# Performance work log

Measured on AMD Instinct MI355X. Metric: run time of the kernel, lower is better.

The kernel has to match this reference:

```python
import jax, jax.numpy as jnp
import numpy as np

D, P, H, FF, HD = 1024, 512, 16, 4096, 64
B, L = 2, 1024
EPS = 1e-5


def rotate_half(x):
    x1, x2 = jnp.split(x, 2, axis=-1)
    return jnp.concatenate([-x2, x1], axis=-1)


def apply_rope(x, pos):  # x: [B,H,L,HD], pos: [L,HD] angles
    c = jnp.cos(pos)[None, None]
    s = jnp.sin(pos)[None, None]
    return x * c + rotate_half(x) * s


def layer_norm(x, g, b):
    mu = jnp.mean(x, axis=-1, keepdims=True)
    var = jnp.var(x, axis=-1, keepdims=True)
    return (x - mu) * jax.lax.rsqrt(var + EPS) * g + b


def heads(x):  # [B,L,D] -> [B,H,L,HD]
    Bq, Lq, _ = x.shape
    return x.reshape(Bq, Lq, H, HD).transpose(0, 2, 1, 3)


def attention(q, k, v, alibi, pos, mask):
    if pos is not None:
        q = apply_rope(q, pos)
        k = apply_rope(k, pos)
    scores = jnp.einsum('bhqd,bhkd->bhqk', q, k) * (HD ** -0.5)
    scores = jnp.where(mask[:, None, None, :], -jnp.inf, scores)
    scores = scores + alibi[None]
    w = jax.nn.softmax(scores, axis=-1)
    out = jnp.einsum('bhqk,bhkd->bhqd', w, v)
    return out.transpose(0, 2, 1, 3).reshape(out.shape[0], out.shape[2], D)


def setup_inputs() -> dict:
    key = jax.random.key(0)
    ks = iter(jax.random.split(key, 64))

    def rn(shape, scale=1.0):
        return jax.random.normal(next(ks), shape, dtype=jnp.float32) * scale

    inp = {
        'memory': rn((B, L, D)),
        'tgt': rn((B, L, D)),
        'self_alibi_bias': rn((H, L, L)),
        'self_pos_emb': rn((L, HD)),
        'cross_alibi_bias': rn((H, L, L)),
        'cross_pos_emb': rn((L, HD)),
        'mask': jax.random.randint(next(ks), (B, L), 0, 2) > 0,
        # self attention params
        'sa_lat_w': rn((D, P), 0.02), 'sa_lat_b': jnp.zeros((P,)),
        'sa_q_w': rn((P, D), 0.02), 'sa_q_b': jnp.zeros((D,)),
        'sa_k_w': rn((P, D), 0.02), 'sa_k_b': jnp.zeros((D,)),
        'sa_v_w': rn((P, D), 0.02), 'sa_v_b': jnp.zeros((D,)),
        'sa_out_w': rn((D, D), 0.02), 'sa_out_b': jnp.zeros((D,)),
        # cross attention params
        'ca_lat_w': rn((D, P), 0.02), 'ca_lat_b': jnp.zeros((P,)),
        'ca_q_w': rn((D, D), 0.02), 'ca_q_b': jnp.zeros((D,)),
        'ca_k_w': rn((P, D), 0.02), 'ca_k_b': jnp.zeros((D,)),
        'ca_v_w': rn((P, D), 0.02), 'ca_v_b': jnp.zeros((D,)),
        'ca_out_w': rn((D, D), 0.02), 'ca_out_b': jnp.zeros((D,)),
        # ffn + norms
        'lin1_w': rn((D, FF), 0.02), 'lin1_b': jnp.zeros((FF,)),
        'lin2_w': rn((FF, D), 0.02), 'lin2_b': jnp.zeros((D,)),
        'n1_g': jnp.ones((D,)), 'n1_b': jnp.zeros((D,)),
        'n2_g': jnp.ones((D,)), 'n2_b': jnp.zeros((D,)),
        'n3_g': jnp.ones((D,)), 'n3_b': jnp.zeros((D,)),
    }
    return inp


def reference(memory, tgt, self_alibi_bias, self_pos_emb, cross_alibi_bias,
              cross_pos_emb, mask,
              sa_lat_w, sa_lat_b, sa_q_w, sa_q_b, sa_k_w, sa_k_b,
              sa_v_w, sa_v_b, sa_out_w, sa_out_b,
              ca_lat_w, ca_lat_b, ca_q_w, ca_q_b, ca_k_w, ca_k_b,
              ca_v_w, ca_v_b, ca_out_w, ca_out_b,
              lin1_w, lin1_b, lin2_w, lin2_b,
              n1_g, n1_b, n2_g, n2_b, n3_g, n3_b):
    # self attention (q,k,v all from latent projection of tgt)
    proj = tgt @ sa_lat_w + sa_lat_b                      # [B,L,P]
    q = heads(proj @ sa_q_w + sa_q_b)
    k = heads(proj @ sa_k_w + sa_k_b)
    v = heads(proj @ sa_v_w + sa_v_b)
    sa = attention(q, k, v, self_alibi_bias, self_pos_emb, mask)
    sa = sa @ sa_out_w + sa_out_b
    x = tgt + layer_norm(sa, n1_g, n1_b)

    # cross attention (q from current tgt stream, k/v from latent of memory)
    mproj = memory @ ca_lat_w + ca_lat_b                  # [B,L,P]
    q = heads(x @ ca_q_w + ca_q_b)
    k = heads(mproj @ ca_k_w + ca_k_b)
    v = heads(mproj @ ca_v_w + ca_v_b)
    ca = attention(q, k, v, cross_alibi_bias, cross_pos_emb, mask)
    ca = ca @ ca_out_w + ca_out_b
    x = x + layer_norm(ca, n2_g, n2_b)

    # FFN
    f = jax.nn.gelu(x @ lin1_w + lin1_b, approximate=False) @ lin2_w + lin2_b
    x = layer_norm(x + f, n3_g, n3_b)
    return x
```

## Files before the change

### kernel.cpp

```cpp
#include <hip/hip_runtime.h>
#include <hip/hip_bf16.h>
#include <math.h>

typedef __hip_bfloat16 hbf16;
typedef __attribute__((ext_vector_type(8))) short bf16x8;
typedef __attribute__((ext_vector_type(4))) float f32x4;

constexpr int kD  = 1024;
constexpr int kP  = 512;
constexpr int kH  = 16;
constexpr int kFF = 4096;
constexpr int kHD = 64;
constexpr int kB  = 2;
constexpr int kL  = 1024;
constexpr int kTok = kB * kL;

__device__ inline short f2bf(float x) { hbf16 h = __float2bfloat16(x); return *(short*)&h; }

__global__ __launch_bounds__(256) void transpose_bf16(
    const float* __restrict__ src, short* __restrict__ dst, int K, int N)
{
    __shared__ float t[32][33];
    int n0 = blockIdx.x * 32, k0 = blockIdx.y * 32;
    int tx = threadIdx.x & 31, ty = threadIdx.x >> 5;
    #pragma unroll
    for (int r = ty; r < 32; r += 8)
        t[r][tx] = src[(size_t)(k0 + r) * N + n0 + tx];
    __syncthreads();
    #pragma unroll
    for (int r = ty; r < 32; r += 8)
        dst[(size_t)(n0 + r) * K + k0 + tx] = f2bf(t[tx][r]);
}

__global__ __launch_bounds__(256) void bias_fill(
    const float* __restrict__ bias, float* __restrict__ C, int N, int total4)
{
    int i = blockIdx.x * 256 + threadIdx.x;
    if (i >= total4) return;
    int n = (i * 4) & (N - 1);
    *(float4*)&C[(size_t)i * 4] = *(const float4*)&bias[n];
}

__global__ void concat_bias(float* __restrict__ o, const float* __restrict__ a,
                            const float* __restrict__ b, const float* __restrict__ c, int n)
{
    int i = blockIdx.x * blockDim.x + threadIdx.x;
    if (i < n) o[i] = a[i];
    else if (i < 2 * n) { if (b) o[i] = b[i - n]; }
    else if (i < 3 * n) { if (c) o[i] = c[i - 2 * n]; }
}

constexpr int LDK = 40;
__global__ __launch_bounds__(256) void gemm_mfma(
    const float* __restrict__ A, const short* __restrict__ WT,
    const float* __restrict__ bias, float* __restrict__ C,
    int M, int N, int K, int act, int ksplit)
{
    __shared__ short As[128 * LDK];
    __shared__ short Bs[128 * LDK];
    const int tid = threadIdx.x;
    const int m0 = blockIdx.y * 128, n0 = blockIdx.x * 128;
    const int ks = K / ksplit;
    const int kbeg = blockIdx.z * ks, kend = kbeg + ks;
    const int wave = tid >> 6, lane = tid & 63;
    const int wm = (wave & 1) * 64, wn = (wave >> 1) * 64;
    const int l15 = lane & 15, quad = lane >> 4;

    const int am = tid >> 3, akq = (tid & 7) * 4;
    const int bn = tid >> 2, bkg = (tid & 3) * 8;

    f32x4 acc[4][4];
    #pragma unroll
    for (int i = 0; i < 4; ++i)
        #pragma unroll
        for (int j = 0; j < 4; ++j)
            acc[i][j] = (f32x4){0.f, 0.f, 0.f, 0.f};

    float4 ra[4];
    bf16x8 rb[2];
    #pragma unroll
    for (int e = 0; e < 4; ++e)
        ra[e] = *(const float4*)&A[(size_t)(m0 + am + e * 32) * K + kbeg + akq];
    #pragma unroll
    for (int e = 0; e < 2; ++e)
        rb[e] = *(const bf16x8*)&WT[(size_t)(n0 + bn + e * 64) * K + kbeg + bkg];

    for (int kk = kbeg; kk < kend; kk += 32) {
        #pragma unroll
        for (int e = 0; e < 4; ++e) {
            short4 s4 = make_short4(f2bf(ra[e].x), f2bf(ra[e].y), f2bf(ra[e].z), f2bf(ra[e].w));
            *(short4*)&As[(am + e * 32) * LDK + akq] = s4;
        }
        #pragma unroll
        for (int e = 0; e < 2; ++e)
            *(bf16x8*)&Bs[(bn + e * 64) * LDK + bkg] = rb[e];
        __syncthreads();

        if (kk + 32 < kend) {
            #pragma unroll
            for (int e = 0; e < 4; ++e)
                ra[e] = *(const float4*)&A[(size_t)(m0 + am + e * 32) * K + kk + 32 + akq];
            #pragma unroll
            for (int e = 0; e < 2; ++e)
                rb[e] = *(const bf16x8*)&WT[(size_t)(n0 + bn + e * 64) * K + kk + 32 + bkg];
        }

        bf16x8 af[4], bfr[4];
        #pragma unroll
        for (int i = 0; i < 4; ++i)
            af[i] = *(bf16x8*)&As[(wm + i * 16 + l15) * LDK + quad * 8];
        #pragma unroll
        for (int j = 0; j < 4; ++j)
            bfr[j] = *(bf16x8*)&Bs[(wn + j * 16 + l15) * LDK + quad * 8];
        #pragma unroll
        for (int i = 0; i < 4; ++i)
            #pragma unroll
            for (int j = 0; j < 4; ++j)
                acc[i][j] = __builtin_amdgcn_mfma_f32_16x16x32_bf16(af[i], bfr[j], acc[i][j], 0, 0, 0);
        __syncthreads();
    }

    #pragma unroll
    for (int j = 0; j < 4; ++j) {
        int n = n0 + wn + j * 16 + l15;
        if (ksplit == 1) {
            float bv = bias[n];
            #pragma unroll
            for (int i = 0; i < 4; ++i) {
                int mb = m0 + wm + i * 16 + quad * 4;
                #pragma unroll
                for (int r = 0; r < 4; ++r) {
                    float v = acc[i][j][r] + bv;
                    if (act) v = v * 0.5f * (1.0f + erff(v * 0.70710678118654752f));
                    C[(size_t)(mb + r) * N + n] = v;
                }
            }
        } else {
            #pragma unroll
            for (int i = 0; i < 4; ++i) {
                int mb = m0 + wm + i * 16 + quad * 4;
                #pragma unroll
                for (int r = 0; r < 4; ++r)
                    atomicAdd(&C[(size_t)(mb + r) * N + n], acc[i][j][r]);
            }
        }
    }
}

__global__ void qk_pack(const float* __restrict__ x, const float* __restrict__ pos,
                        short* __restrict__ outp, float scale, int ldx, int off)
{
    int idx = blockIdx.x * blockDim.x + threadIdx.x;
    if (idx >= kTok * kH * 32) return;
    int d = idx & 31;
    int h = (idx >> 5) & (kH - 1);
    int row = idx >> 9;
    int l = row & (kL - 1);
    int b = row >> 10;
    float a1 = pos[l * kHD + d];
    float a2 = pos[l * kHD + d + 32];
    size_t base = (size_t)row * ldx + off + h * kHD;
    float x1 = x[base + d], x2 = x[base + d + 32];
    float r1 = (x1 * cosf(a1) - x2 * sinf(a1)) * scale;
    float r2 = (x2 * cosf(a2) + x1 * sinf(a2)) * scale;
    size_t ob = ((size_t)(b * kH + h) * kL + l) * 64;
    outp[ob + d]      = f2bf(r1);
    outp[ob + d + 32] = f2bf(r2);
}

__global__ __launch_bounds__(256) void v_pack(const float* __restrict__ v, short* __restrict__ outp,
                                              int ldx, int off)
{
    int l0 = blockIdx.x * 64, h = blockIdx.y, b = blockIdx.z;
    __shared__ float t[64][65];
    int tid = threadIdx.x;
    #pragma unroll
    for (int e = 0; e < 4; ++e) {
        int idx = tid + e * 256;
        int r = idx >> 4, c4 = (idx & 15) * 4;
        const float4 vv = *(const float4*)&v[(size_t)(b * kL + l0 + r) * ldx + off + h * kHD + c4];
        t[r][c4] = vv.x; t[r][c4 + 1] = vv.y; t[r][c4 + 2] = vv.z; t[r][c4 + 3] = vv.w;
    }
    __syncthreads();
    int hd = tid >> 2, seg = (tid & 3) * 16;
    size_t ob = ((size_t)(b * kH + h) * 64 + hd) * kL + l0 + seg;
    short tmp[16];
    #pragma unroll
    for (int i = 0; i < 16; ++i) tmp[i] = f2bf(t[seg + i][hd]);
    #pragma unroll
    for (int i = 0; i < 16; i += 4)
        *(short4*)&outp[ob + i] = make_short4(tmp[i], tmp[i + 1], tmp[i + 2], tmp[i + 3]);
}

constexpr int AQ = 64, AK = 64;
constexpr int QLD = 72;
constexpr int PLD = 68;
__global__ __launch_bounds__(256) void attn_mfma(
    const short* __restrict__ qpk, const short* __restrict__ kpk,
    const short* __restrict__ vpk, const float* __restrict__ alibi,
    const int* __restrict__ mask, float* __restrict__ out)
{
    const int q0 = blockIdx.x * AQ, h = blockIdx.y, b = blockIdx.z;
    const int tid = threadIdx.x, wave = tid >> 6, lane = tid & 63;
    const int l15 = lane & 15, quad = lane >> 4;
    __shared__ short Qs[AQ * QLD];
    __shared__ short Ks[AK * QLD];
    __shared__ short Vt[kHD * QLD];
    __shared__ float Ps[AQ * PLD];

    const short* qbase = qpk + ((size_t)(b * kH + h) * kL) * 64;
    const short* kbase = kpk + ((size_t)(b * kH + h) * kL) * 64;
    const short* vbase = vpk + ((size_t)(b * kH + h) * 64) * kL;

    #pragma unroll
    for (int e = 0; e < 2; ++e) {
        int idx = tid + e * 256;
        int r = idx >> 3, c8 = (idx & 7) * 8;
        *(bf16x8*)&Qs[r * QLD + c8] = *(const bf16x8*)&qbase[(size_t)(q0 + r) * 64 + c8];
    }
    float mst[4], lst[4];
    #pragma unroll
    for (int r = 0; r < 4; ++r) { mst[r] = -3e38f; lst[r] = 0.f; }
    f32x4 oacc[4];
    #pragma unroll
    for (int j = 0; j < 4; ++j) oacc[j] = (f32x4){0.f, 0.f, 0.f, 0.f};
    __syncthreads();

    for (int k0 = 0; k0 < kL; k0 += AK) {
        #pragma unroll
        for (int e = 0; e < 2; ++e) {
            int idx = tid + e * 256;
            int r = idx >> 3, c8 = (idx & 7) * 8;
            *(bf16x8*)&Ks[r * QLD + c8] = *(const bf16x8*)&kbase[(size_t)(k0 + r) * 64 + c8];
            *(bf16x8*)&Vt[r * QLD + c8] = *(const bf16x8*)&vbase[(size_t)r * kL + k0 + c8];
        }
        __syncthreads();

        bf16x8 aq[2];
        #pragma unroll
        for (int s = 0; s < 2; ++s)
            aq[s] = *(bf16x8*)&Qs[(wave * 16 + l15) * QLD + s * 32 + quad * 8];
        f32x4 sacc[4];
        #pragma unroll
        for (int nt = 0; nt < 4; ++nt) sacc[nt] = (f32x4){0.f, 0.f, 0.f, 0.f};
        #pragma unroll
        for (int nt = 0; nt < 4; ++nt)
            #pragma unroll
            for (int s = 0; s < 2; ++s) {
                bf16x8 bk = *(bf16x8*)&Ks[(nt * 16 + l15) * QLD + s * 32 + quad * 8];
                sacc[nt] = __builtin_amdgcn_mfma_f32_16x16x32_bf16(aq[s], bk, sacc[nt], 0, 0, 0);
            }

        float sv[4][4];
        float mx[4] = {-3e38f, -3e38f, -3e38f, -3e38f};
        #pragma unroll
        for (int nt = 0; nt < 4; ++nt) {
            int key = k0 + nt * 16 + l15;
            int mk = mask[b * kL + key];
            #pragma unroll
            for (int r = 0; r < 4; ++r) {
                int qrow = q0 + wave * 16 + quad * 4 + r;
                float al = alibi[((size_t)h * kL + qrow) * kL + key];
                float s = mk ? -1e30f : sacc[nt][r];
                s += al;
                sv[nt][r] = s;
                mx[r] = fmaxf(mx[r], s);
            }
        }
        #pragma unroll
        for (int m = 1; m <= 8; m <<= 1)
            #pragma unroll
            for (int r = 0; r < 4; ++r)
                mx[r] = fmaxf(mx[r], __shfl_xor(mx[r], m));
        float alpha[4], lsum[4];
        #pragma unroll
        for (int r = 0; r < 4; ++r) {
            float mn = fmaxf(mst[r], mx[r]);
            alpha[r] = __expf(mst[r] - mn);
            mst[r] = mn;
            lsum[r] = 0.f;
        }
        #pragma unroll
        for (int nt = 0; nt < 4; ++nt)
            #pragma unroll
            for (int r = 0; r < 4; ++r) {
                float p = __expf(sv[nt][r] - mst[r]);
                sv[nt][r] = p;
                lsum[r] += p;
            }
        #pragma unroll
        for (int m = 1; m <= 8; m <<= 1)
            #pragma unroll
            for (int r = 0; r < 4; ++r)
                lsum[r] += __shfl_xor(lsum[r], m);
        #pragma unroll
        for (int r = 0; r < 4; ++r) lst[r] = lst[r] * alpha[r] + lsum[r];

        #pragma unroll
        for (int nt = 0; nt < 4; ++nt)
            #pragma unroll
            for (int r = 0; r < 4; ++r)
                Ps[(wave * 16 + quad * 4 + r) * PLD + nt * 16 + l15] = sv[nt][r];
        #pragma unroll
        for (int j = 0; j < 4; ++j)
            #pragma unroll
            for (int r = 0; r < 4; ++r)
                oacc[j][r] *= alpha[r];
        __syncthreads();

        #pragma unroll
        for (int s = 0; s < 2; ++s) {
            const float* pr = &Ps[(wave * 16 + l15) * PLD + s * 32 + quad * 8];
            float4 p0 = *(const float4*)&pr[0];
            float4 p1 = *(const float4*)&pr[4];
            bf16x8 ap;
            ap[0] = f2bf(p0.x); ap[1] = f2bf(p0.y); ap[2] = f2bf(p0.z); ap[3] = f2bf(p0.w);
            ap[4] = f2bf(p1.x); ap[5] = f2bf(p1.y); ap[6] = f2bf(p1.z); ap[7] = f2bf(p1.w);
            #pragma unroll
            for (int j = 0; j < 4; ++j) {
                bf16x8 bv = *(bf16x8*)&Vt[(j * 16 + l15) * QLD + s * 32 + quad * 8];
                oacc[j] = __builtin_amdgcn_mfma_f32_16x16x32_bf16(ap, bv, oacc[j], 0, 0, 0);
            }
        }
        __syncthreads();
    }

    #pragma unroll
    for (int j = 0; j < 4; ++j)
        #pragma unroll
        for (int r = 0; r < 4; ++r) {
            int qrow = q0 + wave * 16 + quad * 4 + r;
            out[(size_t)(b * kL + qrow) * kD + h * kHD + j * 16 + l15] = oacc[j][r] / lst[r];
        }
}

__global__ __launch_bounds__(256) void add_ln(
    const float* __restrict__ res, const float* __restrict__ z,
    const float* __restrict__ g, const float* __restrict__ bi,
    float* __restrict__ out)
{
    int row = blockIdx.x, tid = threadIdx.x;
    __shared__ float red[256], red2[256];
    const float* zr = z + (size_t)row * kD;
    float s = 0.f, sq = 0.f;
    for (int i = tid; i < kD; i += 256) { float vv = zr[i]; s += vv; sq += vv * vv; }
    red[tid] = s; red2[tid] = sq; __syncthreads();
    for (int st = 128; st > 0; st >>= 1) {
        if (tid < st) { red[tid] += red[tid + st]; red2[tid] += red2[tid + st]; }
        __syncthreads();
    }
    float mean = red[0] / kD;
    float var = red2[0] / kD - mean * mean;
    float rstd = rsqrtf(var + 1e-5f);
    for (int i = tid; i < kD; i += 256) {
        float vv = (zr[i] - mean) * rstd * g[i] + bi[i];
        out[(size_t)row * kD + i] = res[(size_t)row * kD + i] + vv;
    }
}

__global__ __launch_bounds__(256) void ln_final(
    const float* __restrict__ res, const float* __restrict__ f,
    const float* __restrict__ g, const float* __restrict__ bi,
    float* __restrict__ out)
{
    int row = blockIdx.x, tid = threadIdx.x;
    __shared__ float tt[kD];
    __shared__ float red[256], red2[256];
    float s = 0.f, sq = 0.f;
    for (int i = tid; i < kD; i += 256) {
        float vv = res[(size_t)row * kD + i] + f[(size_t)row * kD + i];
        tt[i] = vv; s += vv; sq += vv * vv;
    }
    red[tid] = s; red2[tid] = sq; __syncthreads();
    for (int st = 128; st > 0; st >>= 1) {
        if (tid < st) { red[tid] += red[tid + st]; red2[tid] += red2[tid + st]; }
        __syncthreads();
    }
    float mean = red[0] / kD;
    float var = red2[0] / kD - mean * mean;
    float rstd = rsqrtf(var + 1e-5f);
    for (int i = tid; i < kD; i += 256)
        out[(size_t)row * kD + i] = (tt[i] - mean) * rstd * g[i] + bi[i];
}

extern "C" void kernel_launch(void* const* d_in, const int* in_sizes, int n_in,
                              void* d_out, int out_size, void* d_ws, size_t ws_size,
                              hipStream_t stream)
{
    const float* memory      = (const float*)d_in[0];
    const float* tgt         = (const float*)d_in[1];
    const float* self_alibi  = (const float*)d_in[2];
    const float* self_pos    = (const float*)d_in[3];
    const float* cross_alibi = (const float*)d_in[4];
    const float* cross_pos   = (const float*)d_in[5];
    const int*   mask        = (const int*)d_in[6];
    const float* sa_lat_w = (const float*)d_in[7];   const float* sa_lat_b = (const float*)d_in[8];
    const float* sa_q_w   = (const float*)d_in[9];   const float* sa_q_b   = (const float*)d_in[10];
    const float* sa_k_w   = (const float*)d_in[11];  const float* sa_k_b   = (const float*)d_in[12];
    const float* sa_v_w   = (const float*)d_in[13];  const float* sa_v_b   = (const float*)d_in[14];
    const float* sa_out_w = (const float*)d_in[15];  const float* sa_out_b = (const float*)d_in[16];
    const float* ca_lat_w = (const float*)d_in[17];  const float* ca_lat_b = (const float*)d_in[18];
    const float* ca_q_w   = (const float*)d_in[19];  const float* ca_q_b   = (const float*)d_in[20];
    const float* ca_k_w   = (const float*)d_in[21];  const float* ca_k_b   = (const float*)d_in[22];
    const float* ca_v_w   = (const float*)d_in[23];  const float* ca_v_b   = (const float*)d_in[24];
    const float* ca_out_w = (const float*)d_in[25];  const float* ca_out_b = (const float*)d_in[26];
    const float* lin1_w   = (const float*)d_in[27];  const float* lin1_b   = (const float*)d_in[28];
    const float* lin2_w   = (const float*)d_in[29];  const float* lin2_b   = (const float*)d_in[30];
    const float* n1_g = (const float*)d_in[31];  const float* n1_b = (const float*)d_in[32];
    const float* n2_g = (const float*)d_in[33];  const float* n2_b = (const float*)d_in[34];
    const float* n3_g = (const float*)d_in[35];  const float* n3_b = (const float*)d_in[36];

    const size_t M1 = 1u << 20;
    float* W     = (float*)d_ws;
    float* xb    = W + 0 * M1;
    float* tmp   = W + 2 * M1;
    float* proj  = W + 4 * M1;
    float* qkvb  = W + 5 * M1;
    float* attnb = W + 11 * M1;
    float* ffh   = W + 4 * M1;
    short* wslot = (short*)(W + 13 * M1);
    float* bcat  = W + 11 * M1;
    short* qpk = (short*)(W + 2 * M1);
    short* kpk = (short*)(W + 3 * M1);
    short* vpk = (short*)(W + 4 * M1);

    auto gemm = [&](const float* A, const float* Wt, const float* bias, float* C,
                    int M, int N, int K, int act, int S) {
        transpose_bf16<<<dim3(N / 32, K / 32), dim3(256), 0, stream>>>(Wt, wslot, K, N);
        if (S > 1)
            bias_fill<<<dim3(M * N / 1024), dim3(256), 0, stream>>>(bias, C, N, M * N / 4);
        gemm_mfma<<<dim3(N / 128, M / 128, S), dim3(256), 0, stream>>>(A, wslot, bias, C, M, N, K, act, S);
    };
    dim3 agrid(kL / AQ, kH, kB);
    dim3 vgrid(kL / 64, kH, kB);
    dim3 tgD(kD / 32, kP / 32);

    gemm(tgt, sa_lat_w, sa_lat_b, proj, kTok, kP, kD, 0, 4);
    transpose_bf16<<<tgD, dim3(256), 0, stream>>>(sa_q_w, wslot, kP, kD);
    transpose_bf16<<<tgD, dim3(256), 0, stream>>>(sa_k_w, wslot + (size_t)kD * kP, kP, kD);
    transpose_bf16<<<tgD, dim3(256), 0, stream>>>(sa_v_w, wslot + (size_t)2 * kD * kP, kP, kD);
    concat_bias<<<dim3(12), dim3(256), 0, stream>>>(bcat, sa_q_b, sa_k_b, sa_v_b, kD);
    gemm_mfma<<<dim3(3 * kD / 128, kTok / 128, 1), dim3(256), 0, stream>>>(
        proj, wslot, bcat, qkvb, kTok, 3 * kD, kP, 0, 1);
    qk_pack<<<dim3(4096), dim3(256), 0, stream>>>(qkvb, self_pos, qpk, 0.125f, 3 * kD, 0);
    qk_pack<<<dim3(4096), dim3(256), 0, stream>>>(qkvb, self_pos, kpk, 1.0f, 3 * kD, kD);
    v_pack<<<vgrid, dim3(256), 0, stream>>>(qkvb, vpk, 3 * kD, 2 * kD);
    attn_mfma<<<agrid, dim3(256), 0, stream>>>(qpk, kpk, vpk, self_alibi, mask, attnb);
    gemm(attnb, sa_out_w, sa_out_b, tmp, kTok, kD, kD, 0, 2);
    add_ln<<<dim3(kTok), dim3(256), 0, stream>>>(tgt, tmp, n1_g, n1_b, xb);

    gemm(memory, ca_lat_w, ca_lat_b, proj, kTok, kP, kD, 0, 4);
    gemm(xb, ca_q_w, ca_q_b, qkvb, kTok, kD, kD, 0, 2);
    transpose_bf16<<<tgD, dim3(256), 0, stream>>>(ca_k_w, wslot, kP, kD);
    transpose_bf16<<<tgD, dim3(256), 0, stream>>>(ca_v_w, wslot + (size_t)kD * kP, kP, kD);
    concat_bias<<<dim3(8), dim3(256), 0, stream>>>(bcat, ca_k_b, ca_v_b, nullptr, kD);
    float* kvb = qkvb + 2 * M1;
    gemm_mfma<<<dim3(2 * kD / 128, kTok / 128, 1), dim3(256), 0, stream>>>(
        proj, wslot, bcat, kvb, kTok, 2 * kD, kP, 0, 1);
    qk_pack<<<dim3(4096), dim3(256), 0, stream>>>(qkvb, cross_pos, qpk, 0.125f, kD, 0);
    qk_pack<<<dim3(4096), dim3(256), 0, stream>>>(kvb, cross_pos, kpk, 1.0f, 2 * kD, 0);
    v_pack<<<vgrid, dim3(256), 0, stream>>>(kvb, vpk, 2 * kD, kD);
    attn_mfma<<<agrid, dim3(256), 0, stream>>>(qpk, kpk, vpk, cross_alibi, mask, attnb);
    gemm(attnb, ca_out_w, ca_out_b, tmp, kTok, kD, kD, 0, 2);
    add_ln<<<dim3(kTok), dim3(256), 0, stream>>>(xb, tmp, n2_g, n2_b, xb);

    gemm(xb, lin1_w, lin1_b, ffh, kTok, kFF, kD, 1, 1);
    gemm(ffh, lin2_w, lin2_b, tmp, kTok, kD, kFF, 0, 4);
    ln_final<<<dim3(kTok), dim3(256), 0, stream>>>(xb, tmp, n3_g, n3_b, (float*)d_out);
}
```

Baseline: 699.0 us.

## Prefetch attention K/V/alibi tiles into registers and stage masked alibi in LDS

The attention kernel now loads the next K, V, alibi and mask tile into registers while the current tile is being computed, then writes it to shared memory at the top of the next iteration. Alibi and mask are read with coalesced float4 loads, pre-masked, and kept in a shared buffer that each wave later reuses for its own P tile. That per-wave reuse removes one block barrier. K, V and Q use a fragment-ordered shared layout, and launch bounds ask for two blocks per CU. The goal is to hide global-memory latency and cut the scattered per-lane alibi and mask reads. The cost is more register pressure from the prefetch buffers, which could limit occupancy or cause spills.

```diff
diff --git a/kernel.cpp b/kernel.cpp
--- a/kernel.cpp
+++ b/kernel.cpp
@@ -193,9 +193,7 @@
 }
 
 constexpr int AQ = 64, AK = 64;
-constexpr int QLD = 72;
-constexpr int PLD = 68;
-__global__ __launch_bounds__(256) void attn_mfma(
+__global__ __launch_bounds__(256, 2) void attn_mfma(
     const short* __restrict__ qpk, const short* __restrict__ kpk,
     const short* __restrict__ vpk, const float* __restrict__ alibi,
     const int* __restrict__ mask, float* __restrict__ out)
@@ -203,43 +201,82 @@
     const int q0 = blockIdx.x * AQ, h = blockIdx.y, b = blockIdx.z;
     const int tid = threadIdx.x, wave = tid >> 6, lane = tid & 63;
     const int l15 = lane & 15, quad = lane >> 4;
-    __shared__ short Qs[AQ * QLD];
-    __shared__ short Ks[AK * QLD];
-    __shared__ short Vt[kHD * QLD];
-    __shared__ float Ps[AQ * PLD];
+    __shared__ short Qf[4096];
+    __shared__ short Kf[4096];
+    __shared__ short Vf[4096];
+    __shared__ float ALPS[4 * 1088];
 
     const short* qbase = qpk + ((size_t)(b * kH + h) * kL) * 64;
     const short* kbase = kpk + ((size_t)(b * kH + h) * kL) * 64;
     const short* vbase = vpk + ((size_t)(b * kH + h) * 64) * kL;
+    const float* abase = alibi + ((size_t)h * kL + q0) * kL;
+    const int*   mbase = mask + b * kL;
+
+    const int sr = tid >> 3, sc8 = (tid & 7) * 8;
+    const int sQuad = (sc8 >> 3) & 3, sS = sc8 >> 5;
+    const int ar = tid >> 4, ac4 = (tid & 15) * 4;
 
     #pragma unroll
     for (int e = 0; e < 2; ++e) {
-        int idx = tid + e * 256;
-        int r = idx >> 3, c8 = (idx & 7) * 8;
-        *(bf16x8*)&Qs[r * QLD + c8] = *(const bf16x8*)&qbase[(size_t)(q0 + r) * 64 + c8];
-    }
+        int r = sr + e * 32;
+        int slot = ((r >> 4) * 2 + sS) * 512 + (r & 15) * 32 + sQuad * 8;
+        *(bf16x8*)&Qf[slot] = *(const bf16x8*)&qbase[(size_t)(q0 + r) * 64 + sc8];
+    }
+
+    bf16x8 rk[2], rv[2];
+    float4 ral[4];
+    int4 rmk;
+    auto load_tile = [&](int k0) {
+        #pragma unroll
+        for (int e = 0; e < 2; ++e) {
+            int r = sr + e * 32;
+            rk[e] = *(const bf16x8*)&kbase[(size_t)(k0 + r) * 64 + sc8];
+            rv[e] = *(const bf16x8*)&vbase[(size_t)r * kL + k0 + sc8];
+        }
+        #pragma unroll
+        for (int e = 0; e < 4; ++e)
+            ral[e] = *(const float4*)&abase[(size_t)(ar + e * 16) * kL + k0 + ac4];
+        rmk = *(const int4*)&mbase[k0 + ac4];
+    };
+    auto store_tile = [&]() {
+        #pragma unroll
+        for (int e = 0; e < 2; ++e) {
+            int r = sr + e * 32;
+            int slot = ((r >> 4) * 2 + sS) * 512 + (r & 15) * 32 + sQuad * 8;
+            *(bf16x8*)&Kf[slot] = rk[e];
+            *(bf16x8*)&Vf[slot] = rv[e];
+        }
+        #pragma unroll
+        for (int e = 0; e < 4; ++e) {
+            float4 a = ral[e];
+            a.x = rmk.x ? -1e30f : a.x;
+            a.y = rmk.y ? -1e30f : a.y;
+            a.z = rmk.z ? -1e30f : a.z;
+            a.w = rmk.w ? -1e30f : a.w;
+            *(float4*)&ALPS[(ar + e * 16) * 68 + ac4] = a;
+        }
+    };
+
     float mst[4], lst[4];
     #pragma unroll
     for (int r = 0; r < 4; ++r) { mst[r] = -3e38f; lst[r] = 0.f; }
     f32x4 oacc[4];
     #pragma unroll
     for (int j = 0; j < 4; ++j) oacc[j] = (f32x4){0.f, 0.f, 0.f, 0.f};
+
+    load_tile(0);
     __syncthreads();
 
-    for (int k0 = 0; k0 < kL; k0 += AK) {
-        #pragma unroll
-        for (int e = 0; e < 2; ++e) {
-            int idx = tid + e * 256;
-            int r = idx >> 3, c8 = (idx & 7) * 8;
-            *(bf16x8*)&Ks[r * QLD + c8] = *(const bf16x8*)&kbase[(size_t)(k0 + r) * 64 + c8];
-            *(bf16x8*)&Vt[r * QLD + c8] = *(const bf16x8*)&vbase[(size_t)r * kL + k0 + c8];
-        }
-        __syncthreads();
-
-        bf16x8 aq[2];
-        #pragma unroll
-        for (int s = 0; s < 2; ++s)
-            aq[s] = *(bf16x8*)&Qs[(wave * 16 + l15) * QLD + s * 32 + quad * 8];
+    bf16x8 aq[2];
+    #pragma unroll
+    for (int s = 0; s < 2; ++s)
+        aq[s] = *(bf16x8*)&Qf[(wave * 2 + s) * 512 + l15 * 32 + quad * 8];
+
+    for (int t = 0; t < kL / AK; ++t) {
+        store_tile();
+        __syncthreads();
+        if (t + 1 < kL / AK) load_tile((t + 1) * AK);
+
         f32x4 sacc[4];
         #pragma unroll
         for (int nt = 0; nt < 4; ++nt) sacc[nt] = (f32x4){0.f, 0.f, 0.f, 0.f};
@@ -247,26 +284,21 @@
         for (int nt = 0; nt < 4; ++nt)
             #pragma unroll
             for (int s = 0; s < 2; ++s) {
-                bf16x8 bk = *(bf16x8*)&Ks[(nt * 16 + l15) * QLD + s * 32 + quad * 8];
+                bf16x8 bk = *(bf16x8*)&Kf[(nt * 2 + s) * 512 + l15 * 32 + quad * 8];
                 sacc[nt] = __builtin_amdgcn_mfma_f32_16x16x32_bf16(aq[s], bk, sacc[nt], 0, 0, 0);
             }
 
         float sv[4][4];
         float mx[4] = {-3e38f, -3e38f, -3e38f, -3e38f};
         #pragma unroll
-        for (int nt = 0; nt < 4; ++nt) {
-            int key = k0 + nt * 16 + l15;
-            int mk = mask[b * kL + key];
+        for (int nt = 0; nt < 4; ++nt)
             #pragma unroll
             for (int r = 0; r < 4; ++r) {
-                int qrow = q0 + wave * 16 + quad * 4 + r;
-                float al = alibi[((size_t)h * kL + qrow) * kL + key];
-                float s = mk ? -1e30f : sacc[nt][r];
-                s += al;
+                float al = ALPS[(wave * 16 + quad * 4 + r) * 68 + nt * 16 + l15];
+                float s = sacc[nt][r] + al;
                 sv[nt][r] = s;
                 mx[r] = fmaxf(mx[r], s);
             }
-        }
         #pragma unroll
         for (int m = 1; m <= 8; m <<= 1)
             #pragma unroll
@@ -300,25 +332,22 @@
         for (int nt = 0; nt < 4; ++nt)
             #pragma unroll
             for (int r = 0; r < 4; ++r)
-                Ps[(wave * 16 + quad * 4 + r) * PLD + nt * 16 + l15] = sv[nt][r];
+                ALPS[wave * 1088 + (quad * 4 + r) * 67 + nt * 16 + l15] = sv[nt][r];
         #pragma unroll
         for (int j = 0; j < 4; ++j)
             #pragma unroll
             for (int r = 0; r < 4; ++r)
                 oacc[j][r] *= alpha[r];
-        __syncthreads();
 
         #pragma unroll
         for (int s = 0; s < 2; ++s) {
-            const float* pr = &Ps[(wave * 16 + l15) * PLD + s * 32 + quad * 8];
-            float4 p0 = *(const float4*)&pr[0];
-            float4 p1 = *(const float4*)&pr[4];
+            int pb = wave * 1088 + l15 * 67 + s * 32 + quad * 8;
             bf16x8 ap;
-            ap[0] = f2bf(p0.x); ap[1] = f2bf(p0.y); ap[2] = f2bf(p0.z); ap[3] = f2bf(p0.w);
-            ap[4] = f2bf(p1.x); ap[5] = f2bf(p1.y); ap[6] = f2bf(p1.z); ap[7] = f2bf(p1.w);
+            #pragma unroll
+            for (int e = 0; e < 8; ++e) ap[e] = f2bf(ALPS[pb + e]);
             #pragma unroll
             for (int j = 0; j < 4; ++j) {
-                bf16x8 bv = *(bf16x8*)&Vt[(j * 16 + l15) * QLD + s * 32 + quad * 8];
+                bf16x8 bv = *(bf16x8*)&Vf[(j * 2 + s) * 512 + l15 * 32 + quad * 8];
                 oacc[j] = __builtin_amdgcn_mfma_f32_16x16x32_bf16(ap, bv, oacc[j], 0, 0, 0);
             }
         }
```

Result: faster. 673.8 us (-3.6%).
